# Optimization experiments

Hardware: AMD Instinct MI355X
Metric: run time of the kernel (lower is better)

## Reference

```python
import jax, jax.numpy as jnp
import numpy as np

N, E, D = 50000, 800000, 128  # nodes, edges, n_feat


def setup_inputs() -> dict:
    key = jax.random.key(0)
    ks = jax.random.split(key, 12)
    scale = 1.0 / np.sqrt(D)

    def w(k):
        return jax.random.normal(k, (D, D), jnp.float32) * scale

    return {
        "h": jax.random.normal(ks[0], (N, D), jnp.float32),
        "src": jax.random.randint(ks[1], (E,), 0, N, jnp.int32),
        "dst": jax.random.randint(ks[2], (E,), 0, N, jnp.int32),
        # skip MLP: Linear -> ELU -> Linear
        "W_skip1": w(ks[3]), "b_skip1": jnp.zeros((D,), jnp.float32),
        "W_skip2": w(ks[4]), "b_skip2": jnp.zeros((D,), jnp.float32),
        # SAGEConv 1 (mean aggregator): fc_self, fc_neigh (bias-free) + shared bias
        "W_self1": w(ks[5]), "W_neigh1": w(ks[6]), "b_conv1": jnp.zeros((D,), jnp.float32),
        # self-interaction MLP
        "W_si1": w(ks[7]), "b_si1": jnp.zeros((D,), jnp.float32),
        "W_si2": w(ks[8]), "b_si2": jnp.zeros((D,), jnp.float32),
        # SAGEConv 2
        "W_self2": w(ks[9]), "W_neigh2": w(ks[10]), "b_conv2": jnp.zeros((D,), jnp.float32),
    }


def _sage_mean(h, src, dst, W_self, W_neigh, b):
    # DGL SAGEConv('mean'): fc_self(h) + fc_neigh(mean over in-neighbors of h_src) + bias
    n = h.shape[0]
    deg = jax.ops.segment_sum(jnp.ones((src.shape[0],), h.dtype), dst, num_segments=n)
    agg = jax.ops.segment_sum(h[src], dst, num_segments=n)  # [N, D] sum of neighbor feats
    agg = agg / jnp.maximum(deg, 1.0)[:, None]  # degree clamp for isolated nodes
    return h @ W_self + agg @ W_neigh + b


def reference(h, src, dst,
              W_skip1, b_skip1, W_skip2, b_skip2,
              W_self1, W_neigh1, b_conv1,
              W_si1, b_si1, W_si2, b_si2,
              W_self2, W_neigh2, b_conv2):
    elu = jax.nn.elu
    h_skip = elu(h @ W_skip1 + b_skip1) @ W_skip2 + b_skip2
    x = elu(_sage_mean(h, src, dst, W_self1, W_neigh1, b_conv1))
    x = elu(elu(x @ W_si1 + b_si1) @ W_si2 + b_si2)
    x = _sage_mean(x, src, dst, W_self2, W_neigh2, b_conv2)
    return h_skip + x
```

## Files before the change

### kernel.cpp

```cpp
#include <hip/hip_runtime.h>
#include <math.h>

#define NN 50000
#define NE 800000
#define NRT 782
#define NT  (NRT * 2)
#define NB  128
#define NPB2 391
#define EPB 2048
#define NBB 391

typedef __attribute__((ext_vector_type(8))) short short8;
typedef __attribute__((ext_vector_type(4))) float floatx4;

#define AS1 __attribute__((address_space(1)))
#define AS3 __attribute__((address_space(3)))

__device__ __forceinline__ unsigned short f2bf(float f) {
    unsigned u = __float_as_uint(f);
    unsigned r = (u + 0x7fff + ((u >> 16) & 1)) >> 16;
    return (unsigned short)r;
}
__device__ __forceinline__ float bf2f(unsigned short h) {
    return __uint_as_float(((unsigned)h) << 16);
}


__global__ __launch_bounds__(256)
void k_prep(const float* __restrict__ h, unsigned short* __restrict__ hB,
            const int* __restrict__ dst, int* __restrict__ bcnt,
            const float* w0, const float* w1, const float* w2, const float* w3,
            const float* w4, const float* w5, const float* w6, const float* w7,
            short* __restrict__ wpk) {
    int bid = blockIdx.x;
    const int t = threadIdx.x;
    if (bid < 3125) {
        int i = (bid * 256 + t) * 8;
        float4 a = *(const float4*)&h[i];
        float4 b = *(const float4*)&h[i + 4];
        short8 v;
        v[0] = (short)f2bf(a.x); v[1] = (short)f2bf(a.y);
        v[2] = (short)f2bf(a.z); v[3] = (short)f2bf(a.w);
        v[4] = (short)f2bf(b.x); v[5] = (short)f2bf(b.y);
        v[6] = (short)f2bf(b.z); v[7] = (short)f2bf(b.w);
        *(short8*)&hB[i] = v;
    } else if (bid < 3125 + NBB) {
        __shared__ int cnt[NB];
        if (t < NB) cnt[t] = 0;
        __syncthreads();
        int base = (bid - 3125) * EPB;
#pragma unroll
        for (int i = 0; i < 8; ++i) {
            int idx = base + i * 256 + t;
            if (idx < NE) atomicAdd(&cnt[dst[idx] / NPB2], 1);
        }
        __syncthreads();
        if (t < NB && cnt[t]) atomicAdd(&bcnt[t], cnt[t]);
    } else {
        int wb = bid - 3125 - NBB;
        const float* W;
        switch (wb) {
            case 0: W = w0; break; case 1: W = w1; break;
            case 2: W = w2; break; case 3: W = w3; break;
            case 4: W = w4; break; case 5: W = w5; break;
            case 6: W = w6; break; default: W = w7; break;
        }
        short* dstp = wpk + (size_t)wb * 16384;
#pragma unroll
        for (int i = 0; i < 8; ++i) {
            int q = t + i * 256;
            int cb = q >> 8, ks = (q >> 6) & 3, lane = q & 63;
            int n = lane & 15, g = lane >> 4;
            int col = cb * 16 + n, krow = ks * 32 + g * 8;
            short8 v;
#pragma unroll
            for (int j = 0; j < 8; ++j)
                v[j] = (short)f2bf(W[(krow + j) * 128 + col]);
            *(short8*)&dstp[q * 8] = v;
        }
    }
}


__global__ void k_bscan(const int* __restrict__ bcnt, int* __restrict__ gcur,
                        int* __restrict__ bstart) {
    __shared__ int s[NB];
    int t = threadIdx.x;
    int c = bcnt[t];
    s[t] = c;
    __syncthreads();
    for (int off = 1; off < NB; off <<= 1) {
        int v = (t >= off) ? s[t - off] : 0;
        __syncthreads();
        s[t] += v;
        __syncthreads();
    }
    int excl = s[t] - c;
    gcur[t] = excl;
    bstart[t] = excl;
    if (t == NB - 1) bstart[NB] = s[NB - 1];
}


__global__ __launch_bounds__(256)
void k_bucket(const int* __restrict__ src, const int* __restrict__ dst,
              int* __restrict__ gcur, int* __restrict__ bsrc, int* __restrict__ bdst) {
    __shared__ int psrc[EPB];
    __shared__ int pdst[EPB];
    __shared__ int cnt[NB];
    __shared__ int ebase[NB];
    __shared__ int gbase[NB];
    const int t = threadIdx.x;
    const int e0 = blockIdx.x * EPB;
    const int M = (e0 + EPB <= NE) ? EPB : (NE - e0);

    if (t < NB) cnt[t] = 0;
    __syncthreads();

    int es[8], ed[8], rank[8];
#pragma unroll
    for (int i = 0; i < 8; ++i) {
        int idx = i * 256 + t;
        if (idx < M) {
            es[i] = src[e0 + idx];
            ed[i] = dst[e0 + idx];
            rank[i] = atomicAdd(&cnt[ed[i] / NPB2], 1);
        }
    }
    __syncthreads();
    if (t < NB) ebase[t] = cnt[t];
    __syncthreads();
    for (int off = 1; off < NB; off <<= 1) {
        int v = 0;
        if (t < NB && t >= off) v = ebase[t - off];
        __syncthreads();
        if (t < NB) ebase[t] += v;
        __syncthreads();
    }
    if (t < NB) ebase[t] -= cnt[t];
    __syncthreads();
#pragma unroll
    for (int i = 0; i < 8; ++i) {
        int idx = i * 256 + t;
        if (idx < M) {
            int b = ed[i] / NPB2;
            int pos = ebase[b] + rank[i];
            psrc[pos] = es[i];
            pdst[pos] = ed[i];
        }
    }
    if (t < NB && cnt[t] > 0) gbase[t] = atomicAdd(&gcur[t], cnt[t]);
    __syncthreads();
#pragma unroll
    for (int i = 0; i < 8; ++i) {
        int idx = i * 256 + t;
        if (idx < M) {
            int d = pdst[idx];
            int b = d / NPB2;
            int gpos = gbase[b] + (idx - ebase[b]);
            bsrc[gpos] = psrc[idx];
            bdst[gpos] = d;
        }
    }
}


template<int DUAL, int DOELU, int OUTF32, int NOBIAS, int BIAS2>
__device__ __forceinline__ void gemm_body(
        int bid,
        const unsigned short* __restrict__ A, const unsigned short* __restrict__ A2,
        const short* __restrict__ Wp, const short* __restrict__ Wp2,
        const float* __restrict__ bias, const float* __restrict__ bias2,
        void* outv, short* sW, short* sA) {
    const int t = threadIdx.x;
    const int wv = t >> 6, lane = t & 63;
    const int rb = bid >> 1, ct = bid & 1;
    const int row0 = rb * 64, col0 = ct * 64;
    const int m = lane & 15, g = lane >> 4;

    floatx4 acc[4];
#pragma unroll
    for (int cb = 0; cb < 4; ++cb) acc[cb] = (floatx4){0.f, 0.f, 0.f, 0.f};

    const int npass = DUAL ? 2 : 1;
    for (int pass = 0; pass < npass; ++pass) {
        const unsigned short* Ac = pass ? A2 : A;
        const short* Wc = (pass ? Wp2 : Wp) + ct * 8192;
        __syncthreads();
#pragma unroll
        for (int i = 0; i < 4; ++i) {
            int cbase = (i * 4 + wv) * 64;
            __builtin_amdgcn_global_load_lds(
                (const AS1 unsigned int*)(Wc + (size_t)(cbase + lane) * 8),
                (AS3 unsigned int*)(sW + cbase * 8), 16, 0, 0);
        }
#pragma unroll
        for (int i = 0; i < 4; ++i) {
            int cbase = (i * 4 + wv) * 64;
            int id = cbase + lane;
            int r = id >> 4, cs = id & 15;
            int rg = row0 + r; if (rg >= NN) rg = NN - 1;
            int csrc = cs ^ (r & 7);
            __builtin_amdgcn_global_load_lds(
                (const AS1 unsigned int*)(Ac + (size_t)rg * 128 + csrc * 8),
                (AS3 unsigned int*)(sA + cbase * 8), 16, 0, 0);
        }
        asm volatile("s_waitcnt vmcnt(0)" ::: "memory");
        __builtin_amdgcn_sched_barrier(0);
        __syncthreads();

        const int r0 = wv * 16;
#pragma unroll
        for (int ks = 0; ks < 4; ++ks) {
            int cxor = (ks * 4 + g) ^ (m & 7);
            short8 af = *(const short8*)&sA[((r0 + m) * 16 + cxor) * 8];
#pragma unroll
            for (int cb = 0; cb < 4; ++cb) {
                short8 bf = *(const short8*)&sW[((cb * 4 + ks) * 64 + lane) * 8];
                acc[cb] = __builtin_amdgcn_mfma_f32_16x16x32_bf16(af, bf, acc[cb], 0, 0, 0);
            }
        }
    }

    const int rowbase = row0 + wv * 16 + g * 4;
#pragma unroll
    for (int cb = 0; cb < 4; ++cb) {
        int C = col0 + cb * 16 + m;
        float bb = NOBIAS ? 0.f : bias[C];
        if (BIAS2) bb += bias2[C];
#pragma unroll
        for (int rr = 0; rr < 4; ++rr) {
            int R = rowbase + rr;
            if (R < NN) {
                size_t idx = (size_t)R * 128 + C;
                float v = acc[cb][rr] + bb;
                if (DOELU) v = (v > 0.f) ? v : expm1f(v);
                if (OUTF32) ((float*)outv)[idx] = v;
                else        ((unsigned short*)outv)[idx] = f2bf(v);
            }
        }
    }
}

template<int DUAL, int DOELU, int OUTF32, int NOBIAS, int BIAS2>
__global__ __launch_bounds__(256)
void k_mm(const unsigned short* __restrict__ A, const unsigned short* __restrict__ A2,
          const short* __restrict__ Wp, const short* __restrict__ Wp2,
          const float* __restrict__ bias, const float* __restrict__ bias2,
          void* outv) {
    __shared__ short sMem[16384];
    gemm_body<DUAL, DOELU, OUTF32, NOBIAS, BIAS2>(blockIdx.x, A, A2, Wp, Wp2,
                                                  bias, bias2, outv, sMem, sMem + 8192);
}


__device__ __forceinline__ void gemm3_body(
        int bid, const unsigned short* __restrict__ A,
        const short* __restrict__ Wn, const short* __restrict__ Ws,
        const short* __restrict__ Wk, const float* __restrict__ bsk1,
        unsigned short* __restrict__ T1, unsigned short* __restrict__ C1,
        unsigned short* __restrict__ S1, short* sW, short* sA) {
    const int t = threadIdx.x;
    const int wv = t >> 6, lane = t & 63;
    const int rb = bid >> 1, ct = bid & 1;
    const int row0 = rb * 64, col0 = ct * 64;
    const int m = lane & 15, g = lane >> 4;

#pragma unroll
    for (int i = 0; i < 4; ++i) {
        int cbase = (i * 4 + wv) * 64;
        int id = cbase + lane;
        int r = id >> 4, cs = id & 15;
        int rg = row0 + r; if (rg >= NN) rg = NN - 1;
        int csrc = cs ^ (r & 7);
        __builtin_amdgcn_global_load_lds(
            (const AS1 unsigned int*)(A + (size_t)rg * 128 + csrc * 8),
            (AS3 unsigned int*)(sA + cbase * 8), 16, 0, 0);
    }

#pragma unroll
    for (int ph = 0; ph < 3; ++ph) {
        if (ph) __syncthreads();
        const short* Wc = (ph == 0 ? Wn : ph == 1 ? Ws : Wk) + ct * 8192;
#pragma unroll
        for (int i = 0; i < 4; ++i) {
            int cbase = (i * 4 + wv) * 64;
            __builtin_amdgcn_global_load_lds(
                (const AS1 unsigned int*)(Wc + (size_t)(cbase + lane) * 8),
                (AS3 unsigned int*)(sW + cbase * 8), 16, 0, 0);
        }
        asm volatile("s_waitcnt vmcnt(0)" ::: "memory");
        __builtin_amdgcn_sched_barrier(0);
        __syncthreads();

        floatx4 acc[4];
#pragma unroll
        for (int cb = 0; cb < 4; ++cb) acc[cb] = (floatx4){0.f, 0.f, 0.f, 0.f};
        const int r0 = wv * 16;
#pragma unroll
        for (int ks = 0; ks < 4; ++ks) {
            int cxor = (ks * 4 + g) ^ (m & 7);
            short8 af = *(const short8*)&sA[((r0 + m) * 16 + cxor) * 8];
#pragma unroll
            for (int cb = 0; cb < 4; ++cb) {
                short8 bf = *(const short8*)&sW[((cb * 4 + ks) * 64 + lane) * 8];
                acc[cb] = __builtin_amdgcn_mfma_f32_16x16x32_bf16(af, bf, acc[cb], 0, 0, 0);
            }
        }

        const int rowbase = row0 + wv * 16 + g * 4;
#pragma unroll
        for (int cb = 0; cb < 4; ++cb) {
            int C = col0 + cb * 16 + m;
            float bb = (ph == 2) ? bsk1[C] : 0.f;
#pragma unroll
            for (int rr = 0; rr < 4; ++rr) {
                int R = rowbase + rr;
                if (R < NN) {
                    size_t idx = (size_t)R * 128 + C;
                    float v = acc[cb][rr] + bb;
                    if (ph == 0)      T1[idx] = f2bf(v);
                    else if (ph == 1) C1[idx] = f2bf(v);
                    else {
                        v = (v > 0.f) ? v : expm1f(v);
                        S1[idx] = f2bf(v);
                    }
                }
            }
        }
    }
}


__global__ __launch_bounds__(256)
void k_mega1(const int* __restrict__ bsrc, const int* __restrict__ bdst,
             const int* __restrict__ bstart, int* __restrict__ row_start,
             int* __restrict__ col_idx,
             const unsigned short* __restrict__ hB, const short* __restrict__ wpk,
             const float* __restrict__ bsk1,
             unsigned short* __restrict__ T1out, unsigned short* __restrict__ C1out,
             unsigned short* __restrict__ S1out) {
    __shared__ short sMem[16384];
    int bid = blockIdx.x;
    if (bid < NB) {
        int* lcur = (int*)sMem;
        int* sc   = lcur + NPB2;
        int* rs   = sc + 512;
        const int t = threadIdx.x;
        const int n0 = bid * NPB2;
        const int n1 = (n0 + NPB2 < NN) ? n0 + NPB2 : NN;
        const int nn = n1 - n0;
        const int w0 = bstart[bid], w1 = bstart[bid + 1];
        for (int i = t; i < nn; i += 256) lcur[i] = 0;
        __syncthreads();
        for (int e = w0 + t; e < w1; e += 256)
            atomicAdd(&lcur[bdst[e] - n0], 1);
        __syncthreads();
        int v0 = (t < nn) ? lcur[t] : 0;
        int v1 = (t + 256 < nn) ? lcur[t + 256] : 0;
        sc[t] = v0; sc[t + 256] = v1;
        __syncthreads();
        for (int off = 1; off < 512; off <<= 1) {
            int a0 = (t >= off) ? sc[t - off] : 0;
            int a1 = (t + 256 >= off) ? sc[t + 256 - off] : 0;
            __syncthreads();
            sc[t] += a0; sc[t + 256] += a1;
            __syncthreads();
        }
        for (int i = t; i < nn; i += 256) {
            int r = w0 + sc[i] - lcur[i];
            rs[i] = r;
            row_start[n0 + i] = r;
            lcur[i] = 0;
        }
        if (bid == 0 && t == 0) row_start[NN] = NE;
        __syncthreads();
        for (int e = w0 + t; e < w1; e += 256) {
            int d = bdst[e] - n0;
            int slot = atomicAdd(&lcur[d], 1);
            col_idx[rs[d] + slot] = bsrc[e];
        }
    } else {
        gemm3_body(bid - NB, hB, wpk + 3 * 16384 , wpk + 2 * 16384 ,
                   wpk , bsk1, T1out, C1out, S1out, sMem, sMem + 8192);
    }
}


__global__ __launch_bounds__(256)
void k_agg1x(const unsigned short* __restrict__ T1, const int* __restrict__ row_start,
             const int* __restrict__ col_idx, const unsigned short* __restrict__ C1,
             const float* __restrict__ bc, unsigned short* __restrict__ X1out) {
    int node = (blockIdx.x * 256 + threadIdx.x) >> 6;
    int lane = threadIdx.x & 63;
    if (node >= NN) return;
    const int grp = lane >> 5, gl = lane & 31;
    const int beg = row_start[node], end = row_start[node + 1];
    const size_t lo = (size_t)(gl * 4);
    float a0 = 0.f, a1 = 0.f, a2 = 0.f, a3 = 0.f;
    int j = beg;
#pragma unroll 1
    for (; j + 8 <= end; j += 8) {
        int s[4];
#pragma unroll
        for (int u = 0; u < 4; ++u) s[u] = col_idx[j + 2 * u + grp];
        uint2 v[4];
#pragma unroll
        for (int u = 0; u < 4; ++u)
            v[u] = *(const uint2*)&T1[(size_t)s[u] * 128 + lo];
#pragma unroll
        for (int u = 0; u < 4; ++u) {
            a0 += bf2f((unsigned short)(v[u].x & 0xffff));
            a1 += bf2f((unsigned short)(v[u].x >> 16));
            a2 += bf2f((unsigned short)(v[u].y & 0xffff));
            a3 += bf2f((unsigned short)(v[u].y >> 16));
        }
    }
#pragma unroll 1
    for (; j < end; j += 2) {
        int e = j + grp;
        if (e < end) {
            int s = col_idx[e];
            uint2 v = *(const uint2*)&T1[(size_t)s * 128 + lo];
            a0 += bf2f((unsigned short)(v.x & 0xffff));
            a1 += bf2f((unsigned short)(v.x >> 16));
            a2 += bf2f((unsigned short)(v.y & 0xffff));
            a3 += bf2f((unsigned short)(v.y >> 16));
        }
    }
    a0 += __shfl_xor(a0, 32);
    a1 += __shfl_xor(a1, 32);
    a2 += __shfl_xor(a2, 32);
    a3 += __shfl_xor(a3, 32);
    if (lane < 32) {
        float inv = 1.0f / fmaxf((float)(end - beg), 1.0f);
        uint2 c = *(const uint2*)&C1[(size_t)node * 128 + lo];
        float4 bv = *(const float4*)&bc[lane * 4];
        float x0 = a0 * inv + bf2f((unsigned short)(c.x & 0xffff)) + bv.x;
        float x1 = a1 * inv + bf2f((unsigned short)(c.x >> 16)) + bv.y;
        float x2 = a2 * inv + bf2f((unsigned short)(c.y & 0xffff)) + bv.z;
        float x3 = a3 * inv + bf2f((unsigned short)(c.y >> 16)) + bv.w;
        x0 = (x0 > 0.f) ? x0 : expm1f(x0);
        x1 = (x1 > 0.f) ? x1 : expm1f(x1);
        x2 = (x2 > 0.f) ? x2 : expm1f(x2);
        x3 = (x3 > 0.f) ? x3 : expm1f(x3);
        uint2 o;
        o.x = (unsigned)f2bf(x0) | ((unsigned)f2bf(x1) << 16);
        o.y = (unsigned)f2bf(x2) | ((unsigned)f2bf(x3) << 16);
        *(uint2*)&X1out[(size_t)node * 128 + lo] = o;
    }
}


__global__ __launch_bounds__(256)
void k_mega3(const unsigned short* __restrict__ X3, const unsigned short* __restrict__ S1,
             const short* __restrict__ wpk, const float* __restrict__ bconv2,
             const float* __restrict__ bsk2, float* __restrict__ outP,
             unsigned short* __restrict__ T2out) {
    __shared__ short sMem[16384];
    int bid = blockIdx.x;
    if (bid < NT) {
        gemm_body<1, 0, 1, 0, 1>(bid, X3, S1, wpk + 6 * 16384, wpk + 1 * 16384,
                                 bconv2, bsk2, outP, sMem, sMem + 8192);
    } else {
        gemm_body<0, 0, 0, 1, 0>(bid - NT, X3, nullptr, wpk + 7 * 16384, nullptr,
                                 nullptr, nullptr, T2out, sMem, sMem + 8192);
    }
}


__global__ __launch_bounds__(256)
void k_aggf(const unsigned short* __restrict__ T2, const int* __restrict__ row_start,
            const int* __restrict__ col_idx, float* __restrict__ out) {
    int node = (blockIdx.x * 256 + threadIdx.x) >> 6;
    int lane = threadIdx.x & 63;
    if (node >= NN) return;
    const int grp = lane >> 5, gl = lane & 31;
    const int beg = row_start[node], end = row_start[node + 1];
    const size_t lo = (size_t)(gl * 4);
    float a0 = 0.f, a1 = 0.f, a2 = 0.f, a3 = 0.f;
    int j = beg;
#pragma unroll 1
    for (; j + 8 <= end; j += 8) {
        int s[4];
#pragma unroll
        for (int u = 0; u < 4; ++u) s[u] = col_idx[j + 2 * u + grp];
        uint2 v[4];
#pragma unroll
        for (int u = 0; u < 4; ++u)
            v[u] = *(const uint2*)&T2[(size_t)s[u] * 128 + lo];
#pragma unroll
        for (int u = 0; u < 4; ++u) {
            a0 += bf2f((unsigned short)(v[u].x & 0xffff));
            a1 += bf2f((unsigned short)(v[u].x >> 16));
            a2 += bf2f((unsigned short)(v[u].y & 0xffff));
            a3 += bf2f((unsigned short)(v[u].y >> 16));
        }
    }
#pragma unroll 1
    for (; j < end; j += 2) {
        int e = j + grp;
        if (e < end) {
            int s = col_idx[e];
            uint2 v = *(const uint2*)&T2[(size_t)s * 128 + lo];
            a0 += bf2f((unsigned short)(v.x & 0xffff));
            a1 += bf2f((unsigned short)(v.x >> 16));
            a2 += bf2f((unsigned short)(v.y & 0xffff));
            a3 += bf2f((unsigned short)(v.y >> 16));
        }
    }
    a0 += __shfl_xor(a0, 32);
    a1 += __shfl_xor(a1, 32);
    a2 += __shfl_xor(a2, 32);
    a3 += __shfl_xor(a3, 32);
    if (lane < 32) {
        float inv = 1.0f / fmaxf((float)(end - beg), 1.0f);
        float4* op = (float4*)&out[(size_t)node * 128 + lo];
        float4 v = *op;
        v.x += a0 * inv; v.y += a1 * inv;
        v.z += a2 * inv; v.w += a3 * inv;
        *op = v;
    }
}


extern "C" void kernel_launch(void* const* d_in, const int* in_sizes, int n_in,
                              void* d_out, int out_size, void* d_ws, size_t ws_size,
                              hipStream_t stream) {
    const float* h        = (const float*)d_in[0];
    const int*   src      = (const int*)d_in[1];
    const int*   dst      = (const int*)d_in[2];
    const float* W_skip1  = (const float*)d_in[3];
    const float* b_skip1  = (const float*)d_in[4];
    const float* W_skip2  = (const float*)d_in[5];
    const float* b_skip2  = (const float*)d_in[6];
    const float* W_self1  = (const float*)d_in[7];
    const float* W_neigh1 = (const float*)d_in[8];
    const float* b_conv1  = (const float*)d_in[9];
    const float* W_si1    = (const float*)d_in[10];
    const float* b_si1    = (const float*)d_in[11];
    const float* W_si2    = (const float*)d_in[12];
    const float* b_si2    = (const float*)d_in[13];
    const float* W_self2  = (const float*)d_in[14];
    const float* W_neigh2 = (const float*)d_in[15];
    const float* b_conv2  = (const float*)d_in[16];
    float* out = (float*)d_out;

    char* ws = (char*)d_ws;
    int* bcnt      = (int*)ws;
    int* gcur      = bcnt + 128;
    int* bstart    = bcnt + 256;
    int* row_start = bcnt + 100096;
    int* col_idx   = bcnt + 150272;
    short* wpk          = (short*)(ws + 3801088);
    unsigned short* hB  = (unsigned short*)(ws + 4063232);
    unsigned short* B1  = (unsigned short*)(ws + 16863232);
    unsigned short* B2  = (unsigned short*)(ws + 29663232);
    int* bsrc           = (int*)(ws + 42463232);
    int* bdst           = (int*)(ws + 45663232);
    unsigned short* C1s = (unsigned short*)d_out;

    hipMemsetAsync(ws, 0, 128 * sizeof(int), stream);

    k_prep<<<3125 + NBB + 8, 256, 0, stream>>>(h, hB, dst, bcnt,
                                               W_skip1, W_skip2, W_self1, W_neigh1,
                                               W_si1, W_si2, W_self2, W_neigh2, wpk);
    k_bscan<<<1, NB, 0, stream>>>(bcnt, gcur, bstart);

    k_bucket<<<NBB, 256, 0, stream>>>(src, dst, gcur, bsrc, bdst);

    k_mega1<<<NB + NT, 256, 0, stream>>>(bsrc, bdst, bstart, row_start, col_idx,
                                         hB, wpk, b_skip1, B1, C1s, B2);

    k_agg1x<<<12500, 256, 0, stream>>>(B1, row_start, col_idx, C1s, b_conv1, hB);

    k_mm<0, 1, 0, 0, 0><<<NT, 256, 0, stream>>>(hB, nullptr, wpk + 4 * 16384, nullptr,
                                                b_si1, nullptr, B1);
    k_mm<0, 1, 0, 0, 0><<<NT, 256, 0, stream>>>(B1, nullptr, wpk + 5 * 16384, nullptr,
                                                b_si2, nullptr, hB);

    k_mega3<<<2 * NT, 256, 0, stream>>>(hB, B2, wpk, b_conv2, b_skip2, out, B1);

    k_aggf<<<12500, 256, 0, stream>>>(B1, row_start, col_idx, out);
}
```

Baseline: 189.2 us.

## Fuse aggregation with self-interaction MLP and final SAGE GEMMs per row tile

```diff
diff --git a/kernel.cpp b/kernel.cpp
--- a/kernel.cpp
+++ b/kernel.cpp
@@ -165,92 +165,112 @@
 }
 
 
-template<int DUAL, int DOELU, int OUTF32, int NOBIAS, int BIAS2>
-__device__ __forceinline__ void gemm_body(
-        int bid,
-        const unsigned short* __restrict__ A, const unsigned short* __restrict__ A2,
-        const short* __restrict__ Wp, const short* __restrict__ Wp2,
-        const float* __restrict__ bias, const float* __restrict__ bias2,
-        void* outv, short* sW, short* sA) {
-    const int t = threadIdx.x;
-    const int wv = t >> 6, lane = t & 63;
-    const int rb = bid >> 1, ct = bid & 1;
-    const int row0 = rb * 64, col0 = ct * 64;
+__device__ __forceinline__ void drain_barrier() {
+    asm volatile("s_waitcnt vmcnt(0)" ::: "memory");
+    __builtin_amdgcn_sched_barrier(0);
+    __syncthreads();
+}
+
+__device__ __forceinline__ void stage_w128(const short* Wc, short* sW, int wv, int lane) {
+#pragma unroll
+    for (int i = 0; i < 8; ++i) {
+        int cbase = (i * 4 + wv) * 64;
+        __builtin_amdgcn_global_load_lds(
+            (const AS1 unsigned int*)(Wc + (size_t)(cbase + lane) * 8),
+            (AS3 unsigned int*)(sW + cbase * 8), 16, 0, 0);
+    }
+}
+
+__device__ __forceinline__ void stage_a64(const unsigned short* Ac, short* sX, int row0,
+                                          int wv, int lane) {
+#pragma unroll
+    for (int i = 0; i < 4; ++i) {
+        int cbase = (i * 4 + wv) * 64;
+        int id = cbase + lane;
+        int r = id >> 4, cs = id & 15;
+        int rg = row0 + r; if (rg >= NN) rg = NN - 1;
+        int csrc = cs ^ (r & 7);
+        __builtin_amdgcn_global_load_lds(
+            (const AS1 unsigned int*)(Ac + (size_t)rg * 128 + csrc * 8),
+            (AS3 unsigned int*)(sX + cbase * 8), 16, 0, 0);
+    }
+}
+
+__device__ __forceinline__ void mm128(const short* sX, const short* sW, int wv, int lane,
+                                      floatx4 acc[8]) {
     const int m = lane & 15, g = lane >> 4;
-
-    floatx4 acc[4];
-#pragma unroll
-    for (int cb = 0; cb < 4; ++cb) acc[cb] = (floatx4){0.f, 0.f, 0.f, 0.f};
-
-    const int npass = DUAL ? 2 : 1;
-    for (int pass = 0; pass < npass; ++pass) {
-        const unsigned short* Ac = pass ? A2 : A;
-        const short* Wc = (pass ? Wp2 : Wp) + ct * 8192;
-        __syncthreads();
-#pragma unroll
-        for (int i = 0; i < 4; ++i) {
-            int cbase = (i * 4 + wv) * 64;
-            __builtin_amdgcn_global_load_lds(
-                (const AS1 unsigned int*)(Wc + (size_t)(cbase + lane) * 8),
-                (AS3 unsigned int*)(sW + cbase * 8), 16, 0, 0);
-        }
-#pragma unroll
-        for (int i = 0; i < 4; ++i) {
-            int cbase = (i * 4 + wv) * 64;
-            int id = cbase + lane;
-            int r = id >> 4, cs = id & 15;
-            int rg = row0 + r; if (rg >= NN) rg = NN - 1;
-            int csrc = cs ^ (r & 7);
-            __builtin_amdgcn_global_load_lds(
-                (const AS1 unsigned int*)(Ac + (size_t)rg * 128 + csrc * 8),
-                (AS3 unsigned int*)(sA + cbase * 8), 16, 0, 0);
-        }
-        asm volatile("s_waitcnt vmcnt(0)" ::: "memory");
-        __builtin_amdgcn_sched_barrier(0);
-        __syncthreads();
-
-        const int r0 = wv * 16;
-#pragma unroll
-        for (int ks = 0; ks < 4; ++ks) {
-            int cxor = (ks * 4 + g) ^ (m & 7);
-            short8 af = *(const short8*)&sA[((r0 + m) * 16 + cxor) * 8];
-#pragma unroll
-            for (int cb = 0; cb < 4; ++cb) {
-                short8 bf = *(const short8*)&sW[((cb * 4 + ks) * 64 + lane) * 8];
-                acc[cb] = __builtin_amdgcn_mfma_f32_16x16x32_bf16(af, bf, acc[cb], 0, 0, 0);
-            }
-        }
-    }
-
-    const int rowbase = row0 + wv * 16 + g * 4;
-#pragma unroll
-    for (int cb = 0; cb < 4; ++cb) {
-        int C = col0 + cb * 16 + m;
-        float bb = NOBIAS ? 0.f : bias[C];
-        if (BIAS2) bb += bias2[C];
+    const int r0 = wv * 16;
+#pragma unroll
+    for (int ks = 0; ks < 4; ++ks) {
+        int slot = (ks * 4 + g) ^ (m & 7);
+        short8 af = *(const short8*)&sX[((r0 + m) * 16 + slot) * 8];
+#pragma unroll
+        for (int cb = 0; cb < 8; ++cb) {
+            short8 bf = *(const short8*)&sW[((cb * 4 + ks) * 64 + lane) * 8];
+            acc[cb] = __builtin_amdgcn_mfma_f32_16x16x32_bf16(af, bf, acc[cb], 0, 0, 0);
+        }
+    }
+}
+
+__device__ __forceinline__ void act_to_lds64(short* sX, const float* bias, int wv, int lane,
+                                             floatx4 acc[8]) {
+    const int m = lane & 15, g = lane >> 4;
+#pragma unroll
+    for (int cb = 0; cb < 8; ++cb) {
+        int C = cb * 16 + m;
+        float bb = bias[C];
 #pragma unroll
         for (int rr = 0; rr < 4; ++rr) {
-            int R = rowbase + rr;
-            if (R < NN) {
-                size_t idx = (size_t)R * 128 + C;
-                float v = acc[cb][rr] + bb;
-                if (DOELU) v = (v > 0.f) ? v : expm1f(v);
-                if (OUTF32) ((float*)outv)[idx] = v;
-                else        ((unsigned short*)outv)[idx] = f2bf(v);
-            }
-        }
-    }
-}
-
-template<int DUAL, int DOELU, int OUTF32, int NOBIAS, int BIAS2>
-__global__ __launch_bounds__(256)
-void k_mm(const unsigned short* __restrict__ A, const unsigned short* __restrict__ A2,
-          const short* __restrict__ Wp, const short* __restrict__ Wp2,
-          const float* __restrict__ bias, const float* __restrict__ bias2,
-          void* outv) {
-    __shared__ short sMem[16384];
-    gemm_body<DUAL, DOELU, OUTF32, NOBIAS, BIAS2>(blockIdx.x, A, A2, Wp, Wp2,
-                                                  bias, bias2, outv, sMem, sMem + 8192);
+            int Rl = wv * 16 + g * 4 + rr;
+            float v = acc[cb][rr] + bb;
+            v = (v > 0.f) ? v : expm1f(v);
+            int slot = (C >> 3) ^ (Rl & 7);
+            sX[(Rl * 16 + slot) * 8 + (C & 7)] = (short)f2bf(v);
+        }
+    }
+#pragma unroll
+    for (int cb = 0; cb < 8; ++cb) acc[cb] = (floatx4){0.f, 0.f, 0.f, 0.f};
+}
+
+__device__ __forceinline__ void gather4(const unsigned short* __restrict__ F,
+                                        const int* __restrict__ col_idx,
+                                        int beg, int end, int grp, size_t lo,
+                                        float& a0, float& a1, float& a2, float& a3) {
+    a0 = a1 = a2 = a3 = 0.f;
+    int j = beg;
+#pragma unroll 1
+    for (; j + 8 <= end; j += 8) {
+        int s[4];
+#pragma unroll
+        for (int u = 0; u < 4; ++u) s[u] = col_idx[j + 2 * u + grp];
+        uint2 v[4];
+#pragma unroll
+        for (int u = 0; u < 4; ++u)
+            v[u] = *(const uint2*)&F[(size_t)s[u] * 128 + lo];
+#pragma unroll
+        for (int u = 0; u < 4; ++u) {
+            a0 += bf2f((unsigned short)(v[u].x & 0xffff));
+            a1 += bf2f((unsigned short)(v[u].x >> 16));
+            a2 += bf2f((unsigned short)(v[u].y & 0xffff));
+            a3 += bf2f((unsigned short)(v[u].y >> 16));
+        }
+    }
+#pragma unroll 1
+    for (; j < end; j += 2) {
+        int e = j + grp;
+        if (e < end) {
+            int s = col_idx[e];
+            uint2 v = *(const uint2*)&F[(size_t)s * 128 + lo];
+            a0 += bf2f((unsigned short)(v.x & 0xffff));
+            a1 += bf2f((unsigned short)(v.x >> 16));
+            a2 += bf2f((unsigned short)(v.y & 0xffff));
+            a3 += bf2f((unsigned short)(v.y >> 16));
+        }
+    }
+    a0 += __shfl_xor(a0, 32);
+    a1 += __shfl_xor(a1, 32);
+    a2 += __shfl_xor(a2, 32);
+    a3 += __shfl_xor(a3, 32);
 }
 
 
@@ -289,9 +309,7 @@
                 (const AS1 unsigned int*)(Wc + (size_t)(cbase + lane) * 8),
                 (AS3 unsigned int*)(sW + cbase * 8), 16, 0, 0);
         }
-        asm volatile("s_waitcnt vmcnt(0)" ::: "memory");
-        __builtin_amdgcn_sched_barrier(0);
-        __syncthreads();
+        drain_barrier();
 
         floatx4 acc[4];
 #pragma unroll
@@ -388,138 +406,141 @@
 
 
 __global__ __launch_bounds__(256)
-void k_agg1x(const unsigned short* __restrict__ T1, const int* __restrict__ row_start,
+void k_fuse1(const unsigned short* __restrict__ T1, const int* __restrict__ row_start,
              const int* __restrict__ col_idx, const unsigned short* __restrict__ C1,
-             const float* __restrict__ bc, unsigned short* __restrict__ X1out) {
-    int node = (blockIdx.x * 256 + threadIdx.x) >> 6;
-    int lane = threadIdx.x & 63;
-    if (node >= NN) return;
+             const float* __restrict__ bc, const short* __restrict__ WpSi1,
+             const short* __restrict__ WpSi2, const float* __restrict__ bs1,
+             const float* __restrict__ bs2, unsigned short* __restrict__ X3out) {
+    __shared__ short sW[16384];
+    __shared__ short sX[8192];
+    const int t = threadIdx.x, wv = t >> 6, lane = t & 63;
+    const int row0 = blockIdx.x * 64;
     const int grp = lane >> 5, gl = lane & 31;
-    const int beg = row_start[node], end = row_start[node + 1];
-    const size_t lo = (size_t)(gl * 4);
-    float a0 = 0.f, a1 = 0.f, a2 = 0.f, a3 = 0.f;
-    int j = beg;
+
+    stage_w128(WpSi1, sW, wv, lane);
+
 #pragma unroll 1
-    for (; j + 8 <= end; j += 8) {
-        int s[4];
-#pragma unroll
-        for (int u = 0; u < 4; ++u) s[u] = col_idx[j + 2 * u + grp];
-        uint2 v[4];
-#pragma unroll
-        for (int u = 0; u < 4; ++u)
-            v[u] = *(const uint2*)&T1[(size_t)s[u] * 128 + lo];
-#pragma unroll
-        for (int u = 0; u < 4; ++u) {
-            a0 += bf2f((unsigned short)(v[u].x & 0xffff));
-            a1 += bf2f((unsigned short)(v[u].x >> 16));
-            a2 += bf2f((unsigned short)(v[u].y & 0xffff));
-            a3 += bf2f((unsigned short)(v[u].y >> 16));
-        }
-    }
+    for (int k = 0; k < 16; ++k) {
+        int node = row0 + wv * 16 + k;
+        if (node < NN) {
+            int beg = row_start[node], end = row_start[node + 1];
+            size_t lo = (size_t)(gl * 4);
+            float a0, a1, a2, a3;
+            gather4(T1, col_idx, beg, end, grp, lo, a0, a1, a2, a3);
+            if (lane < 32) {
+                float inv = 1.0f / fmaxf((float)(end - beg), 1.0f);
+                uint2 c = *(const uint2*)&C1[(size_t)node * 128 + lo];
+                float4 bv = *(const float4*)&bc[gl * 4];
+                float x0 = a0 * inv + bf2f((unsigned short)(c.x & 0xffff)) + bv.x;
+                float x1 = a1 * inv + bf2f((unsigned short)(c.x >> 16)) + bv.y;
+                float x2 = a2 * inv + bf2f((unsigned short)(c.y & 0xffff)) + bv.z;
+                float x3 = a3 * inv + bf2f((unsigned short)(c.y >> 16)) + bv.w;
+                x0 = (x0 > 0.f) ? x0 : expm1f(x0);
+                x1 = (x1 > 0.f) ? x1 : expm1f(x1);
+                x2 = (x2 > 0.f) ? x2 : expm1f(x2);
+                x3 = (x3 > 0.f) ? x3 : expm1f(x3);
+                int Rl = wv * 16 + k;
+                int slot = (gl >> 1) ^ (Rl & 7);
+                unsigned* p = (unsigned*)&sX[(Rl * 16 + slot) * 8 + (gl & 1) * 4];
+                p[0] = (unsigned)f2bf(x0) | ((unsigned)f2bf(x1) << 16);
+                p[1] = (unsigned)f2bf(x2) | ((unsigned)f2bf(x3) << 16);
+            }
+        }
+    }
+
+    floatx4 acc[8];
+#pragma unroll
+    for (int cb = 0; cb < 8; ++cb) acc[cb] = (floatx4){0.f, 0.f, 0.f, 0.f};
+    drain_barrier();
+    mm128(sX, sW, wv, lane, acc);
+
+    __syncthreads();
+    act_to_lds64(sX, bs1, wv, lane, acc);
+    stage_w128(WpSi2, sW, wv, lane);
+    drain_barrier();
+    mm128(sX, sW, wv, lane, acc);
+
+    const int m = lane & 15, g = lane >> 4;
+    const int rowbase = row0 + wv * 16 + g * 4;
+#pragma unroll
+    for (int cb = 0; cb < 8; ++cb) {
+        int C = cb * 16 + m;
+        float bb = bs2[C];
+#pragma unroll
+        for (int rr = 0; rr < 4; ++rr) {
+            int R = rowbase + rr;
+            if (R < NN) {
+                float v = acc[cb][rr] + bb;
+                v = (v > 0.f) ? v : expm1f(v);
+                X3out[(size_t)R * 128 + C] = f2bf(v);
+            }
+        }
+    }
+}
+
+
+__global__ __launch_bounds__(256)
+void k_fuse2(const unsigned short* __restrict__ X3, const unsigned short* __restrict__ S1,
+             const int* __restrict__ row_start, const int* __restrict__ col_idx,
+             const short* __restrict__ WpNeigh2, const short* __restrict__ WpSelf2,
+             const short* __restrict__ WpSk2, const float* __restrict__ bconv2,
+             const float* __restrict__ bsk2, float* __restrict__ out) {
+    __shared__ short sW[16384];
+    __shared__ short sX[8192];
+    const int t = threadIdx.x, wv = t >> 6, lane = t & 63;
+    const int row0 = blockIdx.x * 64;
+    const int grp = lane >> 5, gl = lane & 31;
+
+    stage_w128(WpNeigh2, sW, wv, lane);
+
 #pragma unroll 1
-    for (; j < end; j += 2) {
-        int e = j + grp;
-        if (e < end) {
-            int s = col_idx[e];
-            uint2 v = *(const uint2*)&T1[(size_t)s * 128 + lo];
-            a0 += bf2f((unsigned short)(v.x & 0xffff));
-            a1 += bf2f((unsigned short)(v.x >> 16));
-            a2 += bf2f((unsigned short)(v.y & 0xffff));
-            a3 += bf2f((unsigned short)(v.y >> 16));
-        }
-    }
-    a0 += __shfl_xor(a0, 32);
-    a1 += __shfl_xor(a1, 32);
-    a2 += __shfl_xor(a2, 32);
-    a3 += __shfl_xor(a3, 32);
-    if (lane < 32) {
-        float inv = 1.0f / fmaxf((float)(end - beg), 1.0f);
-        uint2 c = *(const uint2*)&C1[(size_t)node * 128 + lo];
-        float4 bv = *(const float4*)&bc[lane * 4];
-        float x0 = a0 * inv + bf2f((unsigned short)(c.x & 0xffff)) + bv.x;
-        float x1 = a1 * inv + bf2f((unsigned short)(c.x >> 16)) + bv.y;
-        float x2 = a2 * inv + bf2f((unsigned short)(c.y & 0xffff)) + bv.z;
-        float x3 = a3 * inv + bf2f((unsigned short)(c.y >> 16)) + bv.w;
-        x0 = (x0 > 0.f) ? x0 : expm1f(x0);
-        x1 = (x1 > 0.f) ? x1 : expm1f(x1);
-        x2 = (x2 > 0.f) ? x2 : expm1f(x2);
-        x3 = (x3 > 0.f) ? x3 : expm1f(x3);
-        uint2 o;
-        o.x = (unsigned)f2bf(x0) | ((unsigned)f2bf(x1) << 16);
-        o.y = (unsigned)f2bf(x2) | ((unsigned)f2bf(x3) << 16);
-        *(uint2*)&X1out[(size_t)node * 128 + lo] = o;
-    }
-}
-
-
-__global__ __launch_bounds__(256)
-void k_mega3(const unsigned short* __restrict__ X3, const unsigned short* __restrict__ S1,
-             const short* __restrict__ wpk, const float* __restrict__ bconv2,
-             const float* __restrict__ bsk2, float* __restrict__ outP,
-             unsigned short* __restrict__ T2out) {
-    __shared__ short sMem[16384];
-    int bid = blockIdx.x;
-    if (bid < NT) {
-        gemm_body<1, 0, 1, 0, 1>(bid, X3, S1, wpk + 6 * 16384, wpk + 1 * 16384,
-                                 bconv2, bsk2, outP, sMem, sMem + 8192);
-    } else {
-        gemm_body<0, 0, 0, 1, 0>(bid - NT, X3, nullptr, wpk + 7 * 16384, nullptr,
-                                 nullptr, nullptr, T2out, sMem, sMem + 8192);
-    }
-}
-
-
-__global__ __launch_bounds__(256)
-void k_aggf(const unsigned short* __restrict__ T2, const int* __restrict__ row_start,
-            const int* __restrict__ col_idx, float* __restrict__ out) {
-    int node = (blockIdx.x * 256 + threadIdx.x) >> 6;
-    int lane = threadIdx.x & 63;
-    if (node >= NN) return;
-    const int grp = lane >> 5, gl = lane & 31;
-    const int beg = row_start[node], end = row_start[node + 1];
-    const size_t lo = (size_t)(gl * 4);
-    float a0 = 0.f, a1 = 0.f, a2 = 0.f, a3 = 0.f;
-    int j = beg;
-#pragma unroll 1
-    for (; j + 8 <= end; j += 8) {
-        int s[4];
-#pragma unroll
-        for (int u = 0; u < 4; ++u) s[u] = col_idx[j + 2 * u + grp];
-        uint2 v[4];
-#pragma unroll
-        for (int u = 0; u < 4; ++u)
-            v[u] = *(const uint2*)&T2[(size_t)s[u] * 128 + lo];
-#pragma unroll
-        for (int u = 0; u < 4; ++u) {
-            a0 += bf2f((unsigned short)(v[u].x & 0xffff));
-            a1 += bf2f((unsigned short)(v[u].x >> 16));
-            a2 += bf2f((unsigned short)(v[u].y & 0xffff));
-            a3 += bf2f((unsigned short)(v[u].y >> 16));
-        }
-    }
-#pragma unroll 1
-    for (; j < end; j += 2) {
-        int e = j + grp;
-        if (e < end) {
-            int s = col_idx[e];
-            uint2 v = *(const uint2*)&T2[(size_t)s * 128 + lo];
-            a0 += bf2f((unsigned short)(v.x & 0xffff));
-            a1 += bf2f((unsigned short)(v.x >> 16));
-            a2 += bf2f((unsigned short)(v.y & 0xffff));
-            a3 += bf2f((unsigned short)(v.y >> 16));
-        }
-    }
-    a0 += __shfl_xor(a0, 32);
-    a1 += __shfl_xor(a1, 32);
-    a2 += __shfl_xor(a2, 32);
-    a3 += __shfl_xor(a3, 32);
-    if (lane < 32) {
-        float inv = 1.0f / fmaxf((float)(end - beg), 1.0f);
-        float4* op = (float4*)&out[(size_t)node * 128 + lo];
-        float4 v = *op;
-        v.x += a0 * inv; v.y += a1 * inv;
-        v.z += a2 * inv; v.w += a3 * inv;
-        *op = v;
+    for (int k = 0; k < 16; ++k) {
+        int node = row0 + wv * 16 + k;
+        if (node < NN) {
+            int beg = row_start[node], end = row_start[node + 1];
+            size_t lo = (size_t)(gl * 4);
+            float a0, a1, a2, a3;
+            gather4(X3, col_idx, beg, end, grp, lo, a0, a1, a2, a3);
+            if (lane < 32) {
+                float inv = 1.0f / fmaxf((float)(end - beg), 1.0f);
+                int Rl = wv * 16 + k;
+                int slot = (gl >> 1) ^ (Rl & 7);
+                unsigned* p = (unsigned*)&sX[(Rl * 16 + slot) * 8 + (gl & 1) * 4];
+                p[0] = (unsigned)f2bf(a0 * inv) | ((unsigned)f2bf(a1 * inv) << 16);
+                p[1] = (unsigned)f2bf(a2 * inv) | ((unsigned)f2bf(a3 * inv) << 16);
+            }
+        }
+    }
+
+    floatx4 acc[8];
+#pragma unroll
+    for (int cb = 0; cb < 8; ++cb) acc[cb] = (floatx4){0.f, 0.f, 0.f, 0.f};
+    drain_barrier();
+    mm128(sX, sW, wv, lane, acc);
+
+    __syncthreads();
+    stage_a64(X3, sX, row0, wv, lane);
+    stage_w128(WpSelf2, sW, wv, lane);
+    drain_barrier();
+    mm128(sX, sW, wv, lane, acc);
+
+    __syncthreads();
+    stage_a64(S1, sX, row0, wv, lane);
+    stage_w128(WpSk2, sW, wv, lane);
+    drain_barrier();
+    mm128(sX, sW, wv, lane, acc);
+
+    const int m = lane & 15, g = lane >> 4;
+    const int rowbase = row0 + wv * 16 + g * 4;
+#pragma unroll
+    for (int cb = 0; cb < 8; ++cb) {
+        int C = cb * 16 + m;
+        float bb = bconv2[C] + bsk2[C];
+#pragma unroll
+        for (int rr = 0; rr < 4; ++rr) {
+            int R = rowbase + rr;
+            if (R < NN) out[(size_t)R * 128 + C] = acc[cb][rr] + bb;
+        }
     }
 }
 
@@ -572,14 +593,11 @@
     k_mega1<<<NB + NT, 256, 0, stream>>>(bsrc, bdst, bstart, row_start, col_idx,
                                          hB, wpk, b_skip1, B1, C1s, B2);
 
-    k_agg1x<<<12500, 256, 0, stream>>>(B1, row_start, col_idx, C1s, b_conv1, hB);
-
-    k_mm<0, 1, 0, 0, 0><<<NT, 256, 0, stream>>>(hB, nullptr, wpk + 4 * 16384, nullptr,
-                                                b_si1, nullptr, B1);
-    k_mm<0, 1, 0, 0, 0><<<NT, 256, 0, stream>>>(B1, nullptr, wpk + 5 * 16384, nullptr,
-                                                b_si2, nullptr, hB);
-
-    k_mega3<<<2 * NT, 256, 0, stream>>>(hB, B2, wpk, b_conv2, b_skip2, out, B1);
-
-    k_aggf<<<12500, 256, 0, stream>>>(B1, row_start, col_idx, out);
-}
+    k_fuse1<<<NRT, 256, 0, stream>>>(B1, row_start, col_idx, C1s, b_conv1,
+                                     wpk + 4 * 16384, wpk + 5 * 16384,
+                                     b_si1, b_si2, hB);
+
+    k_fuse2<<<NRT, 256, 0, stream>>>(hB, B2, row_start, col_idx,
+                                     wpk + 7 * 16384, wpk + 6 * 16384, wpk + 1 * 16384,
+                                     b_conv2, b_skip2, out);
+}
```

After: 306.0 us. 61.7% more time.

## Aggregate before projecting in second SAGE layer and fuse final GEMMs

Applied to the files above, without the earlier changes.

```diff
diff --git a/kernel.cpp b/kernel.cpp
--- a/kernel.cpp
+++ b/kernel.cpp
@@ -165,12 +165,10 @@
 }
 
 
-template<int DUAL, int DOELU, int OUTF32, int NOBIAS, int BIAS2>
+template<int DOELU, int OUTF32, int NOBIAS>
 __device__ __forceinline__ void gemm_body(
-        int bid,
-        const unsigned short* __restrict__ A, const unsigned short* __restrict__ A2,
-        const short* __restrict__ Wp, const short* __restrict__ Wp2,
-        const float* __restrict__ bias, const float* __restrict__ bias2,
+        int bid, const unsigned short* __restrict__ A,
+        const short* __restrict__ Wp, const float* __restrict__ bias,
         void* outv, short* sW, short* sA) {
     const int t = threadIdx.x;
     const int wv = t >> 6, lane = t & 63;
@@ -182,43 +180,38 @@
 #pragma unroll
     for (int cb = 0; cb < 4; ++cb) acc[cb] = (floatx4){0.f, 0.f, 0.f, 0.f};
 
-    const int npass = DUAL ? 2 : 1;
-    for (int pass = 0; pass < npass; ++pass) {
-        const unsigned short* Ac = pass ? A2 : A;
-        const short* Wc = (pass ? Wp2 : Wp) + ct * 8192;
-        __syncthreads();
-#pragma unroll
-        for (int i = 0; i < 4; ++i) {
-            int cbase = (i * 4 + wv) * 64;
-            __builtin_amdgcn_global_load_lds(
-                (const AS1 unsigned int*)(Wc + (size_t)(cbase + lane) * 8),
-                (AS3 unsigned int*)(sW + cbase * 8), 16, 0, 0);
-        }
-#pragma unroll
-        for (int i = 0; i < 4; ++i) {
-            int cbase = (i * 4 + wv) * 64;
-            int id = cbase + lane;
-            int r = id >> 4, cs = id & 15;
-            int rg = row0 + r; if (rg >= NN) rg = NN - 1;
-            int csrc = cs ^ (r & 7);
-            __builtin_amdgcn_global_load_lds(
-                (const AS1 unsigned int*)(Ac + (size_t)rg * 128 + csrc * 8),
-                (AS3 unsigned int*)(sA + cbase * 8), 16, 0, 0);
-        }
-        asm volatile("s_waitcnt vmcnt(0)" ::: "memory");
-        __builtin_amdgcn_sched_barrier(0);
-        __syncthreads();
-
-        const int r0 = wv * 16;
-#pragma unroll
-        for (int ks = 0; ks < 4; ++ks) {
-            int cxor = (ks * 4 + g) ^ (m & 7);
-            short8 af = *(const short8*)&sA[((r0 + m) * 16 + cxor) * 8];
-#pragma unroll
-            for (int cb = 0; cb < 4; ++cb) {
-                short8 bf = *(const short8*)&sW[((cb * 4 + ks) * 64 + lane) * 8];
-                acc[cb] = __builtin_amdgcn_mfma_f32_16x16x32_bf16(af, bf, acc[cb], 0, 0, 0);
-            }
+    const short* Wc = Wp + ct * 8192;
+#pragma unroll
+    for (int i = 0; i < 4; ++i) {
+        int cbase = (i * 4 + wv) * 64;
+        __builtin_amdgcn_global_load_lds(
+            (const AS1 unsigned int*)(Wc + (size_t)(cbase + lane) * 8),
+            (AS3 unsigned int*)(sW + cbase * 8), 16, 0, 0);
+    }
+#pragma unroll
+    for (int i = 0; i < 4; ++i) {
+        int cbase = (i * 4 + wv) * 64;
+        int id = cbase + lane;
+        int r = id >> 4, cs = id & 15;
+        int rg = row0 + r; if (rg >= NN) rg = NN - 1;
+        int csrc = cs ^ (r & 7);
+        __builtin_amdgcn_global_load_lds(
+            (const AS1 unsigned int*)(A + (size_t)rg * 128 + csrc * 8),
+            (AS3 unsigned int*)(sA + cbase * 8), 16, 0, 0);
+    }
+    asm volatile("s_waitcnt vmcnt(0)" ::: "memory");
+    __builtin_amdgcn_sched_barrier(0);
+    __syncthreads();
+
+    const int r0 = wv * 16;
+#pragma unroll
+    for (int ks = 0; ks < 4; ++ks) {
+        int cxor = (ks * 4 + g) ^ (m & 7);
+        short8 af = *(const short8*)&sA[((r0 + m) * 16 + cxor) * 8];
+#pragma unroll
+        for (int cb = 0; cb < 4; ++cb) {
+            short8 bf = *(const short8*)&sW[((cb * 4 + ks) * 64 + lane) * 8];
+            acc[cb] = __builtin_amdgcn_mfma_f32_16x16x32_bf16(af, bf, acc[cb], 0, 0, 0);
         }
     }
 
@@ -227,7 +220,6 @@
     for (int cb = 0; cb < 4; ++cb) {
         int C = col0 + cb * 16 + m;
         float bb = NOBIAS ? 0.f : bias[C];
-        if (BIAS2) bb += bias2[C];
 #pragma unroll
         for (int rr = 0; rr < 4; ++rr) {
             int R = rowbase + rr;
@@ -242,15 +234,12 @@
     }
 }
 
-template<int DUAL, int DOELU, int OUTF32, int NOBIAS, int BIAS2>
+template<int DOELU, int OUTF32, int NOBIAS>
 __global__ __launch_bounds__(256)
-void k_mm(const unsigned short* __restrict__ A, const unsigned short* __restrict__ A2,
-          const short* __restrict__ Wp, const short* __restrict__ Wp2,
-          const float* __restrict__ bias, const float* __restrict__ bias2,
-          void* outv) {
+void k_mm(const unsigned short* __restrict__ A, const short* __restrict__ Wp,
+          const float* __restrict__ bias, void* outv) {
     __shared__ short sMem[16384];
-    gemm_body<DUAL, DOELU, OUTF32, NOBIAS, BIAS2>(blockIdx.x, A, A2, Wp, Wp2,
-                                                  bias, bias2, outv, sMem, sMem + 8192);
+    gemm_body<DOELU, OUTF32, NOBIAS>(blockIdx.x, A, Wp, bias, outv, sMem, sMem + 8192);
 }
 
 
@@ -327,6 +316,78 @@
                     }
                 }
             }
+        }
+    }
+}
+
+
+__global__ __launch_bounds__(256)
+void k_gfinal(const unsigned short* __restrict__ X3, const unsigned short* __restrict__ AG2,
+              const unsigned short* __restrict__ S1, const short* __restrict__ wpk,
+              const float* __restrict__ bconv2, const float* __restrict__ bsk2,
+              float* __restrict__ out) {
+    __shared__ short sMem[16384];
+    short* sW = sMem;
+    short* sA = sMem + 8192;
+    const int t = threadIdx.x;
+    const int wv = t >> 6, lane = t & 63;
+    const int rb = blockIdx.x >> 1, ct = blockIdx.x & 1;
+    const int row0 = rb * 64, col0 = ct * 64;
+    const int m = lane & 15, g = lane >> 4;
+
+    floatx4 acc[4];
+#pragma unroll
+    for (int cb = 0; cb < 4; ++cb) acc[cb] = (floatx4){0.f, 0.f, 0.f, 0.f};
+
+#pragma unroll
+    for (int ph = 0; ph < 3; ++ph) {
+        if (ph) __syncthreads();
+        const unsigned short* Ac = (ph == 0) ? X3 : (ph == 1) ? AG2 : S1;
+        const short* Wc = wpk + (ph == 0 ? 6 : ph == 1 ? 7 : 1) * 16384 + ct * 8192;
+#pragma unroll
+        for (int i = 0; i < 4; ++i) {
+            int cbase = (i * 4 + wv) * 64;
+            __builtin_amdgcn_global_load_lds(
+                (const AS1 unsigned int*)(Wc + (size_t)(cbase + lane) * 8),
+                (AS3 unsigned int*)(sW + cbase * 8), 16, 0, 0);
+        }
+#pragma unroll
+        for (int i = 0; i < 4; ++i) {
+            int cbase = (i * 4 + wv) * 64;
+            int id = cbase + lane;
+            int r = id >> 4, cs = id & 15;
+            int rg = row0 + r; if (rg >= NN) rg = NN - 1;
+            int csrc = cs ^ (r & 7);
+            __builtin_amdgcn_global_load_lds(
+                (const AS1 unsigned int*)(Ac + (size_t)rg * 128 + csrc * 8),
+                (AS3 unsigned int*)(sA + cbase * 8), 16, 0, 0);
+        }
+        asm volatile("s_waitcnt vmcnt(0)" ::: "memory");
+        __builtin_amdgcn_sched_barrier(0);
+        __syncthreads();
+
+        const int r0 = wv * 16;
+#pragma unroll
+        for (int ks = 0; ks < 4; ++ks) {
+            int cxor = (ks * 4 + g) ^ (m & 7);
+            short8 af = *(const short8*)&sA[((r0 + m) * 16 + cxor) * 8];
+#pragma unroll
+            for (int cb = 0; cb < 4; ++cb) {
+                short8 bf = *(const short8*)&sW[((cb * 4 + ks) * 64 + lane) * 8];
+                acc[cb] = __builtin_amdgcn_mfma_f32_16x16x32_bf16(af, bf, acc[cb], 0, 0, 0);
+            }
+        }
+    }
+
+    const int rowbase = row0 + wv * 16 + g * 4;
+#pragma unroll
+    for (int cb = 0; cb < 4; ++cb) {
+        int C = col0 + cb * 16 + m;
+        float bb = bconv2[C] + bsk2[C];
+#pragma unroll
+        for (int rr = 0; rr < 4; ++rr) {
+            int R = rowbase + rr;
+            if (R < NN) out[(size_t)R * 128 + C] = acc[cb][rr] + bb;
         }
     }
 }
@@ -435,7 +496,7 @@
     if (lane < 32) {
         float inv = 1.0f / fmaxf((float)(end - beg), 1.0f);
         uint2 c = *(const uint2*)&C1[(size_t)node * 128 + lo];
-        float4 bv = *(const float4*)&bc[lane * 4];
+        float4 bv = *(const float4*)&bc[gl * 4];
         float x0 = a0 * inv + bf2f((unsigned short)(c.x & 0xffff)) + bv.x;
         float x1 = a1 * inv + bf2f((unsigned short)(c.x >> 16)) + bv.y;
         float x2 = a2 * inv + bf2f((unsigned short)(c.y & 0xffff)) + bv.z;
@@ -453,25 +514,8 @@
 
 
 __global__ __launch_bounds__(256)
-void k_mega3(const unsigned short* __restrict__ X3, const unsigned short* __restrict__ S1,
-             const short* __restrict__ wpk, const float* __restrict__ bconv2,
-             const float* __restrict__ bsk2, float* __restrict__ outP,
-             unsigned short* __restrict__ T2out) {
-    __shared__ short sMem[16384];
-    int bid = blockIdx.x;
-    if (bid < NT) {
-        gemm_body<1, 0, 1, 0, 1>(bid, X3, S1, wpk + 6 * 16384, wpk + 1 * 16384,
-                                 bconv2, bsk2, outP, sMem, sMem + 8192);
-    } else {
-        gemm_body<0, 0, 0, 1, 0>(bid - NT, X3, nullptr, wpk + 7 * 16384, nullptr,
-                                 nullptr, nullptr, T2out, sMem, sMem + 8192);
-    }
-}
-
-
-__global__ __launch_bounds__(256)
-void k_aggf(const unsigned short* __restrict__ T2, const int* __restrict__ row_start,
-            const int* __restrict__ col_idx, float* __restrict__ out) {
+void k_agg2(const unsigned short* __restrict__ X3, const int* __restrict__ row_start,
+            const int* __restrict__ col_idx, unsigned short* __restrict__ AG2out) {
     int node = (blockIdx.x * 256 + threadIdx.x) >> 6;
     int lane = threadIdx.x & 63;
     if (node >= NN) return;
@@ -488,7 +532,7 @@
         uint2 v[4];
 #pragma unroll
         for (int u = 0; u < 4; ++u)
-            v[u] = *(const uint2*)&T2[(size_t)s[u] * 128 + lo];
+            v[u] = *(const uint2*)&X3[(size_t)s[u] * 128 + lo];
 #pragma unroll
         for (int u = 0; u < 4; ++u) {
             a0 += bf2f((unsigned short)(v[u].x & 0xffff));
@@ -502,7 +546,7 @@
         int e = j + grp;
         if (e < end) {
             int s = col_idx[e];
-            uint2 v = *(const uint2*)&T2[(size_t)s * 128 + lo];
+            uint2 v = *(const uint2*)&X3[(size_t)s * 128 + lo];
             a0 += bf2f((unsigned short)(v.x & 0xffff));
             a1 += bf2f((unsigned short)(v.x >> 16));
             a2 += bf2f((unsigned short)(v.y & 0xffff));
@@ -515,11 +559,10 @@
     a3 += __shfl_xor(a3, 32);
     if (lane < 32) {
         float inv = 1.0f / fmaxf((float)(end - beg), 1.0f);
-        float4* op = (float4*)&out[(size_t)node * 128 + lo];
-        float4 v = *op;
-        v.x += a0 * inv; v.y += a1 * inv;
-        v.z += a2 * inv; v.w += a3 * inv;
-        *op = v;
+        uint2 o;
+        o.x = (unsigned)f2bf(a0 * inv) | ((unsigned)f2bf(a1 * inv) << 16);
+        o.y = (unsigned)f2bf(a2 * inv) | ((unsigned)f2bf(a3 * inv) << 16);
+        *(uint2*)&AG2out[(size_t)node * 128 + lo] = o;
     }
 }
 
@@ -574,12 +617,10 @@
 
     k_agg1x<<<12500, 256, 0, stream>>>(B1, row_start, col_idx, C1s, b_conv1, hB);
 
-    k_mm<0, 1, 0, 0, 0><<<NT, 256, 0, stream>>>(hB, nullptr, wpk + 4 * 16384, nullptr,
-                                                b_si1, nullptr, B1);
-    k_mm<0, 1, 0, 0, 0><<<NT, 256, 0, stream>>>(B1, nullptr, wpk + 5 * 16384, nullptr,
-                                                b_si2, nullptr, hB);
-
-    k_mega3<<<2 * NT, 256, 0, stream>>>(hB, B2, wpk, b_conv2, b_skip2, out, B1);
-
-    k_aggf<<<12500, 256, 0, stream>>>(B1, row_start, col_idx, out);
-}
+    k_mm<1, 0, 0><<<NT, 256, 0, stream>>>(hB, wpk + 4 * 16384, b_si1, B1);
+    k_mm<1, 0, 0><<<NT, 256, 0, stream>>>(B1, wpk + 5 * 16384, b_si2, hB);
+
+    k_agg2<<<12500, 256, 0, stream>>>(hB, row_start, col_idx, B1);
+
+    k_gfinal<<<NT, 256, 0, stream>>>(hB, B1, B2, wpk, b_conv2, b_skip2, out);
+}
```

New measurement: 184.4 us. -2.6%, faster.
